# Optimization experiments

Measured on AMD Instinct MI355X. Metric: run time of the kernel, lower is better.

The kernel has to match this reference:

```python
import jax, jax.numpy as jnp
import numpy as np

EMBED_DIM = 128
NUM_HEADS = 4
HEAD_DIM = EMBED_DIM // NUM_HEADS


def setup_inputs() -> dict:
    key = jax.random.key(0)
    ks = jax.random.split(key, 12)
    B, N, D = 4, 4096, EMBED_DIM
    s = 1.0 / np.sqrt(D)
    inp = {
        "query": jax.random.normal(ks[0], (B, N, D), dtype=jnp.float32),
        "key": jax.random.normal(ks[1], (B, N, D), dtype=jnp.float32),
        "value": jax.random.normal(ks[2], (B, N, D), dtype=jnp.float32),
        "Wq": jax.random.uniform(ks[3], (D, D), jnp.float32, -s, s),
        "bq": jax.random.uniform(ks[4], (D,), jnp.float32, -s, s),
        "Wk": jax.random.uniform(ks[5], (D, D), jnp.float32, -s, s),
        "bk": jax.random.uniform(ks[6], (D,), jnp.float32, -s, s),
        "Wv": jax.random.uniform(ks[7], (D, D), jnp.float32, -s, s),
        "bv": jax.random.uniform(ks[8], (D,), jnp.float32, -s, s),
        "Wo": jax.random.uniform(ks[9], (D, D), jnp.float32, -s, s),
        "bo": jax.random.uniform(ks[10], (D,), jnp.float32, -s, s),
    }
    return inp


def reference(query, key, value, Wq, bq, Wk, bk, Wv, bv, Wo, bo):
    B, N, D = query.shape
    H, Dh = NUM_HEADS, HEAD_DIM
    scale = Dh ** -0.5
    # Linear projections (torch Linear: x @ W.T + b), split heads -> [B, H, N, Dh]
    Q = (query @ Wq.T + bq).reshape(B, N, H, Dh).transpose(0, 2, 1, 3)
    K = (key @ Wk.T + bk).reshape(B, N, H, Dh).transpose(0, 2, 1, 3)
    V = (value @ Wv.T + bv).reshape(B, N, H, Dh).transpose(0, 2, 1, 3)
    # Attention scores [B, H, N, N]
    scores = jnp.einsum('bhqd,bhkd->bhqk', Q, K) * scale
    attn = jax.nn.softmax(scores, axis=-1)
    ctx = jnp.einsum('bhqk,bhkd->bhqd', attn, V)  # [B, H, N, Dh]
    ctx = ctx.transpose(0, 2, 1, 3).reshape(B, N, D)
    return ctx @ Wo.T + bo
```

## Files before the change

kernel.cpp:

```cpp
#include <hip/hip_runtime.h>
#include <hip/hip_bf16.h>

#define N_SEQ 4096
#define DIM   128
#define NH    4
#define DH    32
#define BATCH 4

#define QSCALE 0.25503495870989204f

typedef __bf16 bf16x8 __attribute__((ext_vector_type(8)));
typedef __bf16 bf16x2 __attribute__((ext_vector_type(2)));
typedef __bf16 bf16x4 __attribute__((ext_vector_type(4)));
typedef float  f32x4  __attribute__((ext_vector_type(4)));

#define MFMA(a, b, c) __builtin_amdgcn_mfma_f32_16x16x32_bf16((a), (b), (c), 0, 0, 0)

static __device__ __forceinline__ bf16x8 cvt8(const float* __restrict__ p) {
    const float4* f4 = reinterpret_cast<const float4*>(p);
    float4 a = f4[0], b = f4[1];
    bf16x8 r;
    r[0] = (__bf16)a.x; r[1] = (__bf16)a.y; r[2] = (__bf16)a.z; r[3] = (__bf16)a.w;
    r[4] = (__bf16)b.x; r[5] = (__bf16)b.y; r[6] = (__bf16)b.z; r[7] = (__bf16)b.w;
    return r;
}

static __device__ __forceinline__ f32x4 exp4(f32x4 s) {
    f32x4 r;
    r[0] = __builtin_amdgcn_exp2f(s[0]);
    r[1] = __builtin_amdgcn_exp2f(s[1]);
    r[2] = __builtin_amdgcn_exp2f(s[2]);
    r[3] = __builtin_amdgcn_exp2f(s[3]);
    return r;
}

static __device__ __forceinline__ bf16x8 pack8(f32x4 a, f32x4 b) {
    bf16x8 o;
    o[0] = (__bf16)a[0]; o[1] = (__bf16)a[1];
    o[2] = (__bf16)a[2]; o[3] = (__bf16)a[3];
    o[4] = (__bf16)b[0]; o[5] = (__bf16)b[1];
    o[6] = (__bf16)b[2]; o[7] = (__bf16)b[3];
    return o;
}

__global__ __launch_bounds__(256) void proj_qkv(
    const float* __restrict__ xq, const float* __restrict__ xk, const float* __restrict__ xv,
    const float* __restrict__ Wq, const float* __restrict__ Wk, const float* __restrict__ Wv,
    const float* __restrict__ bq, const float* __restrict__ bk, const float* __restrict__ bv,
    __bf16* __restrict__ Qs, __bf16* __restrict__ Kb, __bf16* __restrict__ Vt)
{
    __shared__ __align__(16) char wlds[34816];
    const int z = blockIdx.z;
    const float* x    = (z == 0) ? xq : ((z == 1) ? xk : xv);
    const float* Wf   = (z == 0) ? Wq : ((z == 1) ? Wk : Wv);
    const float* bias = (z == 0) ? bq : ((z == 1) ? bk : bv);
    const int b    = blockIdx.y;
    const int tid  = threadIdx.x;
    const int wave = tid >> 6, lane = tid & 63;
    const int quad = lane >> 4, l15 = lane & 15;
    const int n0   = blockIdx.x * 64 + wave * 16;

    {
        const int r = tid >> 1, half = tid & 1;
        const float* wsrc = Wf + r * DIM + half * 64;
        char* wdst = wlds + r * 272 + half * 128;
        #pragma unroll
        for (int i = 0; i < 8; i++)
            *(bf16x8*)(wdst + i * 16) = cvt8(wsrc + i * 8);
    }

    bf16x8 a[4];
    const float* xrow = x + (b * N_SEQ + n0 + l15) * DIM + quad * 8;
    a[0] = cvt8(xrow);      a[1] = cvt8(xrow + 32);
    a[2] = cvt8(xrow + 64); a[3] = cvt8(xrow + 96);
    __syncthreads();

    const int n = n0 + l15;
    for (int t = 0; t < 8; t++) {
        const char* wr = wlds + (t * 16 + l15) * 272 + quad * 16;
        bf16x8 w0 = *(const bf16x8*)(wr);
        bf16x8 w1 = *(const bf16x8*)(wr + 64);
        bf16x8 w2 = *(const bf16x8*)(wr + 128);
        bf16x8 w3 = *(const bf16x8*)(wr + 192);

        f32x4 acc = {0.f, 0.f, 0.f, 0.f};
        acc = MFMA(w0, a[0], acc);
        acc = MFMA(w1, a[1], acc);
        acc = MFMA(w2, a[2], acc);
        acc = MFMA(w3, a[3], acc);

        const int d0 = t * 16 + quad * 4;
        if (z == 0) {
            const int h = d0 >> 5, dh0 = d0 & 31;
            bf16x4 q4;
            #pragma unroll
            for (int r = 0; r < 4; r++)
                q4[r] = (__bf16)((acc[r] + bias[d0 + r]) * QSCALE);
            *(bf16x4*)(Qs + ((b * NH + h) * N_SEQ + n) * DH + dh0) = q4;
        } else if (z == 1) {
            const int h = d0 >> 5, dh0 = d0 & 31;
            bf16x4 k4;
            #pragma unroll
            for (int r = 0; r < 4; r++)
                k4[r] = (__bf16)(acc[r] + bias[d0 + r]);
            *(bf16x4*)(Kb + ((b * NH + h) * N_SEQ + n) * DH + dh0) = k4;
        } else {
            const int nl = n & 63;
            const int np = (n & ~63) | (nl & 35) | ((nl & 12) << 1) | ((nl & 16) >> 2);
            #pragma unroll
            for (int r = 0; r < 4; r++) {
                const int d = d0 + r, h = d >> 5, dh = d & 31;
                Vt[((b * NH + h) * DH + dh) * N_SEQ + np] = (__bf16)(acc[r] + bias[d]);
            }
        }
    }
}

__global__ __launch_bounds__(256, 2) void flash_attn(
    const __bf16* __restrict__ Qs, const __bf16* __restrict__ Kb,
    const __bf16* __restrict__ Vt, __bf16* __restrict__ ctxb)
{
    __shared__ __align__(16) char smem[57344];
    char* const Kbase = smem;
    char* const Vbase = smem + 20480;
    char* const Pbase = smem + 38912;

    const int bid  = blockIdx.x;
    const int bh   = bid & 15;
    const int qc   = bid >> 4;
    const int tid  = threadIdx.x;
    const int wave = tid >> 6, lane = tid & 63;
    const int quad = lane >> 4, l15 = lane & 15;
    const int qh   = wave & 1, kh = wave >> 1;
    const int n0   = qc * 128 + qh * 64;

    const __bf16* Qp = Qs + (bh * N_SEQ + n0) * DH;
    bf16x8 qf[4];
    #pragma unroll
    for (int q = 0; q < 4; q++)
        qf[q] = *(const bf16x8*)(Qp + (q * 16 + l15) * DH + quad * 8);

    const int r_ = tid >> 2, c_ = tid & 3;
    const __bf16* gK = Kb + (size_t)bh * N_SEQ * DH + r_ * DH + c_ * 8;
    const __bf16* gV = Vt + ((size_t)bh * DH + (tid >> 3)) * N_SEQ + (tid & 7) * 8;
    const int kofsK = r_ * 80 + c_ * 16;
    const int kofsV = (tid >> 3) * 144 + (tid & 7) * 16;
    const int KH = 2048;

    {
        bf16x8 k0 = *(const bf16x8*)(gK);
        bf16x8 k1 = *(const bf16x8*)(gK + (size_t)KH * DH);
        bf16x8 v0 = *(const bf16x8*)(gV);
        bf16x8 v1 = *(const bf16x8*)(gV + KH);
        *(bf16x8*)(Kbase + kofsK)          = k0;
        *(bf16x8*)(Kbase + 10240 + kofsK)  = k1;
        *(bf16x8*)(Vbase + kofsV)          = v0;
        *(bf16x8*)(Vbase + 9216 + kofsV)   = v1;
    }
    __syncthreads();

    char* const Kme = Kbase + kh * 10240;
    char* const Vme = Vbase + kh * 9216;

    f32x4 c[4][2];
    #pragma unroll
    for (int q = 0; q < 4; q++) { c[q][0] = f32x4{0.f,0.f,0.f,0.f}; c[q][1] = f32x4{0.f,0.f,0.f,0.f}; }
    float l[4] = {0.f, 0.f, 0.f, 0.f};
    const f32x4 z4 = {0.f,0.f,0.f,0.f};

    for (int kb = 0; kb < KH / 64; kb++) {
        const int cur = kb & 1;
        const char* Kc = Kme + cur * 5120;
        const char* Vc = Vme + cur * 4608;

        const int kn = (kb + 1) & (KH / 64 - 1);
        bf16x8 krn0 = *(const bf16x8*)(gK + (size_t)(kn * 64) * DH);
        bf16x8 krn1 = *(const bf16x8*)(gK + (size_t)(KH + kn * 64) * DH);
        bf16x8 vrn0 = *(const bf16x8*)(gV + kn * 64);
        bf16x8 vrn1 = *(const bf16x8*)(gV + KH + kn * 64);

        bf16x8 kf0 = *(const bf16x8*)(Kc + l15 * 80 + quad * 16);
        bf16x8 kf1 = *(const bf16x8*)(Kc + (16 + l15) * 80 + quad * 16);
        bf16x8 kf2 = *(const bf16x8*)(Kc + (32 + l15) * 80 + quad * 16);
        bf16x8 kf3 = *(const bf16x8*)(Kc + (48 + l15) * 80 + quad * 16);

        bf16x8 pf[4][2];
        #pragma unroll
        for (int q = 0; q < 4; q++) {
            f32x4 sa = MFMA(kf0, qf[q], z4);
            f32x4 sb = MFMA(kf1, qf[q], z4);
            f32x4 sc = MFMA(kf2, qf[q], z4);
            f32x4 sd = MFMA(kf3, qf[q], z4);
            f32x4 ea = exp4(sa), eb = exp4(sb), ec = exp4(sc), ed = exp4(sd);
            l[q] += ((ea[0]+ea[1])+(ea[2]+ea[3])) + ((eb[0]+eb[1])+(eb[2]+eb[3]))
                  + ((ec[0]+ec[1])+(ec[2]+ec[3])) + ((ed[0]+ed[1])+(ed[2]+ed[3]));
            pf[q][0] = pack8(ea, eb);
            pf[q][1] = pack8(ec, ed);
        }

        bf16x8 vf00 = *(const bf16x8*)(Vc + l15 * 144 + quad * 16);
        bf16x8 vf10 = *(const bf16x8*)(Vc + (16 + l15) * 144 + quad * 16);
        bf16x8 vf01 = *(const bf16x8*)(Vc + l15 * 144 + 64 + quad * 16);
        bf16x8 vf11 = *(const bf16x8*)(Vc + (16 + l15) * 144 + 64 + quad * 16);

        #pragma unroll
        for (int q = 0; q < 4; q++) {
            c[q][0] = MFMA(vf00, pf[q][0], c[q][0]);
            c[q][1] = MFMA(vf10, pf[q][0], c[q][1]);
            c[q][0] = MFMA(vf01, pf[q][1], c[q][0]);
            c[q][1] = MFMA(vf11, pf[q][1], c[q][1]);
        }

        *(bf16x8*)(Kbase + (cur ^ 1) * 5120 + kofsK)          = krn0;
        *(bf16x8*)(Kbase + 10240 + (cur ^ 1) * 5120 + kofsK)  = krn1;
        *(bf16x8*)(Vbase + (cur ^ 1) * 4608 + kofsV)          = vrn0;
        *(bf16x8*)(Vbase + 9216 + (cur ^ 1) * 4608 + kofsV)   = vrn1;
        __syncthreads();
    }

    #pragma unroll
    for (int q = 0; q < 4; q++) {
        l[q] += __shfl_xor(l[q], 16);
        l[q] += __shfl_xor(l[q], 32);
    }

    char* const Pme = Pbase + qh * 9216 + lane * 144;
    if (kh == 1) {
        #pragma unroll
        for (int q = 0; q < 4; q++) {
            *(f32x4*)(Pme + (q * 2 + 0) * 16) = c[q][0];
            *(f32x4*)(Pme + (q * 2 + 1) * 16) = c[q][1];
        }
        f32x4 lv = {l[0], l[1], l[2], l[3]};
        *(f32x4*)(Pme + 128) = lv;
    }
    __syncthreads();
    if (kh == 0) {
        f32x4 lp = *(const f32x4*)(Pme + 128);
        const int b = bh >> 2, h = bh & 3;
        #pragma unroll
        for (int q = 0; q < 4; q++) {
            c[q][0] += *(const f32x4*)(Pme + (q * 2 + 0) * 16);
            c[q][1] += *(const f32x4*)(Pme + (q * 2 + 1) * 16);
            const float inv = 1.0f / (l[q] + lp[q]);
            const int qg = n0 + q * 16 + l15;
            __bf16* dst = ctxb + ((size_t)(b * N_SEQ + qg)) * DIM + h * DH + quad * 4;
            #pragma unroll
            for (int dt = 0; dt < 2; dt++) {
                f32x4 cc = c[q][dt];
                bf16x2 e0 = {(__bf16)(cc[0] * inv), (__bf16)(cc[1] * inv)};
                bf16x2 e1 = {(__bf16)(cc[2] * inv), (__bf16)(cc[3] * inv)};
                *(bf16x2*)(dst + dt * 16)     = e0;
                *(bf16x2*)(dst + dt * 16 + 2) = e1;
            }
        }
    }
}

__global__ __launch_bounds__(256) void out_proj(
    const __bf16* __restrict__ ctxb, const float* __restrict__ Wo,
    const float* __restrict__ bo, float* __restrict__ out)
{
    __shared__ __align__(16) char wlds[34816];
    const int b    = blockIdx.y;
    const int tid  = threadIdx.x;
    const int wave = tid >> 6, lane = tid & 63;
    const int quad = lane >> 4, l15 = lane & 15;
    const int n0   = blockIdx.x * 64 + wave * 16;

    {
        const int r = tid >> 1, half = tid & 1;
        const float* wsrc = Wo + r * DIM + half * 64;
        char* wdst = wlds + r * 272 + half * 128;
        #pragma unroll
        for (int i = 0; i < 8; i++)
            *(bf16x8*)(wdst + i * 16) = cvt8(wsrc + i * 8);
    }

    bf16x8 a[4];
    const __bf16* crow = ctxb + (b * N_SEQ + n0 + l15) * DIM + quad * 8;
    a[0] = *(const bf16x8*)(crow);
    a[1] = *(const bf16x8*)(crow + 32);
    a[2] = *(const bf16x8*)(crow + 64);
    a[3] = *(const bf16x8*)(crow + 96);
    __syncthreads();

    const int n = n0 + l15;
    for (int t = 0; t < 8; t++) {
        const char* wr = wlds + (t * 16 + l15) * 272 + quad * 16;
        bf16x8 w0 = *(const bf16x8*)(wr);
        bf16x8 w1 = *(const bf16x8*)(wr + 64);
        bf16x8 w2 = *(const bf16x8*)(wr + 128);
        bf16x8 w3 = *(const bf16x8*)(wr + 192);

        f32x4 acc = {0.f, 0.f, 0.f, 0.f};
        acc = MFMA(w0, a[0], acc);
        acc = MFMA(w1, a[1], acc);
        acc = MFMA(w2, a[2], acc);
        acc = MFMA(w3, a[3], acc);

        const int d0 = t * 16 + quad * 4;
        float4 o;
        o.x = acc[0] + bo[d0];
        o.y = acc[1] + bo[d0 + 1];
        o.z = acc[2] + bo[d0 + 2];
        o.w = acc[3] + bo[d0 + 3];
        *(float4*)(out + (b * N_SEQ + n) * DIM + d0) = o;
    }
}

extern "C" void kernel_launch(void* const* d_in, const int* in_sizes, int n_in,
                              void* d_out, int out_size, void* d_ws, size_t ws_size,
                              hipStream_t stream)
{
    const float* query = (const float*)d_in[0];
    const float* key   = (const float*)d_in[1];
    const float* value = (const float*)d_in[2];
    const float* Wq = (const float*)d_in[3];
    const float* bq = (const float*)d_in[4];
    const float* Wk = (const float*)d_in[5];
    const float* bk = (const float*)d_in[6];
    const float* Wv = (const float*)d_in[7];
    const float* bv = (const float*)d_in[8];
    const float* Wo = (const float*)d_in[9];
    const float* bo = (const float*)d_in[10];
    float* out = (float*)d_out;

    char* ws = (char*)d_ws;
    const size_t e = (size_t)BATCH * N_SEQ * DIM;
    __bf16* Qs   = (__bf16*)(ws);
    __bf16* Kb   = (__bf16*)(ws + 2 * e);
    __bf16* Vt   = (__bf16*)(ws + 4 * e);
    __bf16* ctxb = (__bf16*)(ws + 6 * e);

    proj_qkv<<<dim3(64, BATCH, 3), 256, 0, stream>>>(
        query, key, value, Wq, Wk, Wv, bq, bk, bv, Qs, Kb, Vt);
    flash_attn<<<dim3(512), 256, 0, stream>>>(Qs, Kb, Vt, ctxb);
    out_proj<<<dim3(64, BATCH), 256, 0, stream>>>(ctxb, Wo, bo, out);
}
```

Baseline: 150.2 us.

## Split attention key range across four waves per query half with 512-thread blocks

The flash attention block grows from 4 to 8 waves, so each query half is now served by four waves, each covering a quarter of the keys instead of a half. LDS holds four K/V double-buffered slices, and each thread loads two of them. At the end, three partial accumulators and row sums are reduced through shared memory. The aim is more resident waves per CU to hide memory and MFMA latency, at the cost of more LDS per block and a larger cross-wave reduction.

```diff
diff --git a/kernel.cpp b/kernel.cpp
--- a/kernel.cpp
+++ b/kernel.cpp
@@ -116,14 +116,13 @@
     }
 }
 
-__global__ __launch_bounds__(256, 2) void flash_attn(
+__global__ __launch_bounds__(512, 4) void flash_attn(
     const __bf16* __restrict__ Qs, const __bf16* __restrict__ Kb,
     const __bf16* __restrict__ Vt, __bf16* __restrict__ ctxb)
 {
-    __shared__ __align__(16) char smem[57344];
+    __shared__ __align__(16) char smem[77824];
     char* const Kbase = smem;
-    char* const Vbase = smem + 20480;
-    char* const Pbase = smem + 38912;
+    char* const Vbase = smem + 40960;
 
     const int bid  = blockIdx.x;
     const int bh   = bid & 15;
@@ -133,6 +132,7 @@
     const int quad = lane >> 4, l15 = lane & 15;
     const int qh   = wave & 1, kh = wave >> 1;
     const int n0   = qc * 128 + qh * 64;
+    const int KH   = 1024;
 
     const __bf16* Qp = Qs + (bh * N_SEQ + n0) * DH;
     bf16x8 qf[4];
@@ -140,22 +140,27 @@
     for (int q = 0; q < 4; q++)
         qf[q] = *(const bf16x8*)(Qp + (q * 16 + l15) * DH + quad * 8);
 
-    const int r_ = tid >> 2, c_ = tid & 3;
-    const __bf16* gK = Kb + (size_t)bh * N_SEQ * DH + r_ * DH + c_ * 8;
-    const __bf16* gV = Vt + ((size_t)bh * DH + (tid >> 3)) * N_SEQ + (tid & 7) * 8;
+    const int t8  = tid & 255, khA = tid >> 8;
+    const int r_  = t8 >> 2,  c_  = t8 & 3;
+    const __bf16* gK = Kb + (size_t)bh * N_SEQ * DH + (khA * KH + r_) * DH + c_ * 8;
+    const __bf16* gV = Vt + ((size_t)bh * DH + (t8 >> 3)) * N_SEQ + khA * KH + (t8 & 7) * 8;
     const int kofsK = r_ * 80 + c_ * 16;
-    const int kofsV = (tid >> 3) * 144 + (tid & 7) * 16;
-    const int KH = 2048;
+    const int kofsV = (t8 >> 3) * 144 + (t8 & 7) * 16;
+    const int kStep2 = 2 * KH * DH;
+    char* const KldsA = Kbase + khA * 10240 + kofsK;
+    char* const KldsB = Kbase + (khA + 2) * 10240 + kofsK;
+    char* const VldsA = Vbase + khA * 9216 + kofsV;
+    char* const VldsB = Vbase + (khA + 2) * 9216 + kofsV;
 
     {
         bf16x8 k0 = *(const bf16x8*)(gK);
-        bf16x8 k1 = *(const bf16x8*)(gK + (size_t)KH * DH);
+        bf16x8 k1 = *(const bf16x8*)(gK + kStep2);
         bf16x8 v0 = *(const bf16x8*)(gV);
-        bf16x8 v1 = *(const bf16x8*)(gV + KH);
-        *(bf16x8*)(Kbase + kofsK)          = k0;
-        *(bf16x8*)(Kbase + 10240 + kofsK)  = k1;
-        *(bf16x8*)(Vbase + kofsV)          = v0;
-        *(bf16x8*)(Vbase + 9216 + kofsV)   = v1;
+        bf16x8 v1 = *(const bf16x8*)(gV + 2 * KH);
+        *(bf16x8*)(KldsA) = k0;
+        *(bf16x8*)(KldsB) = k1;
+        *(bf16x8*)(VldsA) = v0;
+        *(bf16x8*)(VldsB) = v1;
     }
     __syncthreads();
 
@@ -175,9 +180,9 @@
 
         const int kn = (kb + 1) & (KH / 64 - 1);
         bf16x8 krn0 = *(const bf16x8*)(gK + (size_t)(kn * 64) * DH);
-        bf16x8 krn1 = *(const bf16x8*)(gK + (size_t)(KH + kn * 64) * DH);
+        bf16x8 krn1 = *(const bf16x8*)(gK + (size_t)(kn * 64) * DH + kStep2);
         bf16x8 vrn0 = *(const bf16x8*)(gV + kn * 64);
-        bf16x8 vrn1 = *(const bf16x8*)(gV + KH + kn * 64);
+        bf16x8 vrn1 = *(const bf16x8*)(gV + 2 * KH + kn * 64);
 
         bf16x8 kf0 = *(const bf16x8*)(Kc + l15 * 80 + quad * 16);
         bf16x8 kf1 = *(const bf16x8*)(Kc + (16 + l15) * 80 + quad * 16);
@@ -211,10 +216,10 @@
             c[q][1] = MFMA(vf11, pf[q][1], c[q][1]);
         }
 
-        *(bf16x8*)(Kbase + (cur ^ 1) * 5120 + kofsK)          = krn0;
-        *(bf16x8*)(Kbase + 10240 + (cur ^ 1) * 5120 + kofsK)  = krn1;
-        *(bf16x8*)(Vbase + (cur ^ 1) * 4608 + kofsV)          = vrn0;
-        *(bf16x8*)(Vbase + 9216 + (cur ^ 1) * 4608 + kofsV)   = vrn1;
+        *(bf16x8*)(KldsA + (cur ^ 1) * 5120) = krn0;
+        *(bf16x8*)(KldsB + (cur ^ 1) * 5120) = krn1;
+        *(bf16x8*)(VldsA + (cur ^ 1) * 4608) = vrn0;
+        *(bf16x8*)(VldsB + (cur ^ 1) * 4608) = vrn1;
         __syncthreads();
     }
 
@@ -224,25 +229,33 @@
         l[q] += __shfl_xor(l[q], 32);
     }
 
-    char* const Pme = Pbase + qh * 9216 + lane * 144;
-    if (kh == 1) {
+    if (kh != 0) {
+        char* dst = smem + ((qh * 3 + (kh - 1)) * 64 + lane) * 144;
         #pragma unroll
         for (int q = 0; q < 4; q++) {
-            *(f32x4*)(Pme + (q * 2 + 0) * 16) = c[q][0];
-            *(f32x4*)(Pme + (q * 2 + 1) * 16) = c[q][1];
+            *(f32x4*)(dst + (q * 2 + 0) * 16) = c[q][0];
+            *(f32x4*)(dst + (q * 2 + 1) * 16) = c[q][1];
         }
         f32x4 lv = {l[0], l[1], l[2], l[3]};
-        *(f32x4*)(Pme + 128) = lv;
+        *(f32x4*)(dst + 128) = lv;
     }
     __syncthreads();
     if (kh == 0) {
-        f32x4 lp = *(const f32x4*)(Pme + 128);
+        #pragma unroll
+        for (int m = 0; m < 3; m++) {
+            const char* src = smem + ((qh * 3 + m) * 64 + lane) * 144;
+            #pragma unroll
+            for (int q = 0; q < 4; q++) {
+                c[q][0] += *(const f32x4*)(src + (q * 2 + 0) * 16);
+                c[q][1] += *(const f32x4*)(src + (q * 2 + 1) * 16);
+            }
+            f32x4 lp = *(const f32x4*)(src + 128);
+            l[0] += lp[0]; l[1] += lp[1]; l[2] += lp[2]; l[3] += lp[3];
+        }
         const int b = bh >> 2, h = bh & 3;
         #pragma unroll
         for (int q = 0; q < 4; q++) {
-            c[q][0] += *(const f32x4*)(Pme + (q * 2 + 0) * 16);
-            c[q][1] += *(const f32x4*)(Pme + (q * 2 + 1) * 16);
-            const float inv = 1.0f / (l[q] + lp[q]);
+            const float inv = 1.0f / l[q];
             const int qg = n0 + q * 16 + l15;
             __bf16* dst = ctxb + ((size_t)(b * N_SEQ + qg)) * DIM + h * DH + quad * 4;
             #pragma unroll
@@ -335,6 +348,6 @@
 
     proj_qkv<<<dim3(64, BATCH, 3), 256, 0, stream>>>(
         query, key, value, Wq, Wk, Wv, bq, bk, bv, Qs, Kb, Vt);
-    flash_attn<<<dim3(512), 256, 0, stream>>>(Qs, Kb, Vt, ctxb);
+    flash_attn<<<dim3(512), 512, 0, stream>>>(Qs, Kb, Vt, ctxb);
     out_proj<<<dim3(64, BATCH), 256, 0, stream>>>(ctxb, Wo, bo, out);
 }
```

New measurement: 195.2 us. 30.0% more time.
